# Kernel tuning notes

Hardware: AMD Instinct MI355X
Metric: run time of the kernel (lower is better)

Reference implementation:

```python
import jax, jax.numpy as jnp
import numpy as np

N_NODES = 100000
N_EDGES = 1000000
D_MODEL = 128
EDGE_DIM = 64
LN_EPS = 1e-5


def _layernorm(x, gamma, beta, eps=LN_EPS):
    mu = jnp.mean(x, axis=-1, keepdims=True)
    var = jnp.var(x, axis=-1, keepdims=True)
    return (x - mu) * jax.lax.rsqrt(var + eps) * gamma + beta


def setup_inputs() -> dict:
    key = jax.random.key(0)
    ks = jax.random.split(key, 12)
    std = 1.0 / np.sqrt(D_MODEL)
    stde = 1.0 / np.sqrt(EDGE_DIM)
    return {
        "x_src": jax.random.normal(ks[0], (N_NODES, D_MODEL), jnp.float32),
        "x_dst": jax.random.normal(ks[1], (N_NODES, D_MODEL), jnp.float32),
        "edge_attr": jax.random.normal(ks[2], (N_EDGES, EDGE_DIM), jnp.float32),
        "edge_index": jax.random.randint(ks[3], (2, N_EDGES), 0, N_NODES, jnp.int32),
        # params
        "W_src": jax.random.uniform(ks[4], (D_MODEL, D_MODEL), jnp.float32, -std, std),
        "W_dst": jax.random.uniform(ks[5], (D_MODEL, D_MODEL), jnp.float32, -std, std),
        "b_dst": jnp.zeros((D_MODEL,), jnp.float32),
        "Wg1": jax.random.uniform(ks[6], (EDGE_DIM, D_MODEL), jnp.float32, -stde, stde),
        "bg1": jnp.zeros((D_MODEL,), jnp.float32),
        "Wg2": jax.random.uniform(ks[7], (D_MODEL, 1), jnp.float32, -std, std),
        "bg2": jnp.zeros((1,), jnp.float32),
        "gamma": jnp.ones((D_MODEL,), jnp.float32),
        "beta": jnp.zeros((D_MODEL,), jnp.float32),
    }


def reference(x_src, x_dst, edge_attr, edge_index,
              W_src, W_dst, b_dst, Wg1, bg1, Wg2, bg2, gamma, beta):
    s, d = edge_index[0], edge_index[1]
    n = x_dst.shape[0]
    # gather + linear (no bias): [E, D]
    msg = x_src[s] @ W_src
    # edge gate MLP: Linear -> gelu -> Linear (no norm, eval so no dropout)
    h = jax.nn.gelu(edge_attr @ Wg1 + bg1, approximate=False)
    gate = jax.nn.sigmoid(h @ Wg2 + bg2)  # [E, 1]
    msg = msg * gate
    # scatter-add aggregate + mean by in-degree (clamped at 1)
    out = jax.ops.segment_sum(msg, d, num_segments=n)
    deg = jax.ops.segment_sum(jnp.ones((msg.shape[0],), msg.dtype), d, num_segments=n)
    out = out / jnp.clip(deg, 1.0)[:, None]
    # residual-like combine, layernorm, gelu
    out = _layernorm(out + x_dst @ W_dst + b_dst, gamma, beta)
    return jax.nn.gelu(out, approximate=False)
```

## Files before the change

### kernel.cpp

```cpp
#include <hip/hip_runtime.h>
#include <hip/hip_fp16.h>
#include <math.h>

#define N_NODES 100000
#define N_EDGES 1000000
#define D_MODEL 128
#define EDGE_DIM 64
#define SCHUNK 250
#define NSB 400

typedef short bf16x8 __attribute__((ext_vector_type(8)));
typedef float f32x4 __attribute__((ext_vector_type(4)));

__device__ __forceinline__ short f2bf(float f) {
    union { float f; unsigned u; } v; v.f = f;
    unsigned r = v.u + 0x7FFFu + ((v.u >> 16) & 1u);
    return (short)(r >> 16);
}
__device__ __forceinline__ float gelu_fast(float x) {
    float t = 0.7978845608028654f * x * (1.0f + 0.044715f * x * x);
    float e = __expf(2.0f * t);
    return x * (1.0f - __builtin_amdgcn_rcpf(e + 1.0f));
}
__device__ __forceinline__ float sigmoid_fast(float x) {
    return __builtin_amdgcn_rcpf(1.0f + __expf(-x));
}
__device__ __forceinline__ float bflo(unsigned v) { return __uint_as_float(v << 16); }
__device__ __forceinline__ float bfhi(unsigned v) { return __uint_as_float(v & 0xFFFF0000u); }

__global__ __launch_bounds__(256) void k_prep(
    const float* __restrict__ Ws, const float* __restrict__ Wd,
    const float* __restrict__ Wg1, short* __restrict__ frag,
    int* __restrict__ deg)
{
    int b = blockIdx.x;
    if (b >= 20) {
        int i = (b - 20) * 256 + threadIdx.x;
        if (i < N_NODES) deg[i] = 0;
        return;
    }
    int g = b * 256 + threadIdx.x;
    if (g >= 5120) return;
    const float* W; short* T; int q;
    if (g < 2048)      { W = Ws;  T = frag;         q = g; }
    else if (g < 4096) { W = Wd;  T = frag + 16384; q = g - 2048; }
    else               { W = Wg1; T = frag + 32768; q = g - 4096; }
    int ls = q & 63, nt = (q >> 6) & 7, kb = q >> 9;
    int col = nt * 16 + (ls & 15);
    int k0 = kb * 32 + (ls >> 4) * 8;
    bf16x8 v;
    #pragma unroll
    for (int e = 0; e < 8; ++e) v[e] = f2bf(W[(k0 + e) * D_MODEL + col]);
    *reinterpret_cast<bf16x8*>(T + (size_t)q * 8) = v;
}

__global__ void k_deg(const int* __restrict__ dst, int* __restrict__ deg, int* __restrict__ rank) {
    int e = blockIdx.x * 256 + threadIdx.x;
    if (e < N_EDGES) rank[e] = atomicAdd(&deg[dst[e]], 1);
}

__global__ __launch_bounds__(256) void k_scan1(const int* __restrict__ deg, int* __restrict__ bsum) {
    __shared__ int s[256];
    int tid = threadIdx.x;
    int i = blockIdx.x * SCHUNK + tid;
    int v = (tid < SCHUNK && i < N_NODES) ? deg[i] : 0;
    s[tid] = v; __syncthreads();
    for (int off = 128; off > 0; off >>= 1) {
        if (tid < off) s[tid] += s[tid + off];
        __syncthreads();
    }
    if (tid == 0) bsum[blockIdx.x] = s[0];
}
__global__ __launch_bounds__(512) void k_scan2(const int* __restrict__ bsum, int* __restrict__ boff) {
    __shared__ int s[512];
    int tid = threadIdx.x;
    int v = (tid < NSB) ? bsum[tid] : 0;
    s[tid] = v; __syncthreads();
    for (int off = 1; off < 512; off <<= 1) {
        int t = (tid >= off) ? s[tid - off] : 0;
        __syncthreads();
        s[tid] += t;
        __syncthreads();
    }
    if (tid < NSB) boff[tid] = s[tid] - v;
}
__global__ __launch_bounds__(256) void k_scan3(const int* __restrict__ deg, const int* __restrict__ boff,
                                               int* __restrict__ rstart) {
    __shared__ int s[256];
    int tid = threadIdx.x;
    int i = blockIdx.x * SCHUNK + tid;
    int v = (tid < SCHUNK && i < N_NODES) ? deg[i] : 0;
    s[tid] = v; __syncthreads();
    for (int off = 1; off < 256; off <<= 1) {
        int t = (tid >= off) ? s[tid - off] : 0;
        __syncthreads();
        s[tid] += t;
        __syncthreads();
    }
    int excl = s[tid] - v;
    if (tid < SCHUNK && i < N_NODES) {
        rstart[i] = boff[blockIdx.x] + excl;
        if (i == N_NODES - 1) rstart[N_NODES] = boff[blockIdx.x] + excl + v;
    }
}

__global__ __launch_bounds__(256, 3) void k_node_linear(
    const float* __restrict__ x_src, const float* __restrict__ x_dst,
    const short* __restrict__ WsrcF, const short* __restrict__ WdstF,
    const float* __restrict__ b_dst,
    short* __restrict__ ysrc, short* __restrict__ z_bf)
{
    __shared__ __align__(16) short Bf[4][8][64][8];
    const int tid = threadIdx.x;
    const int lane = tid & 63;
    const int wid = tid >> 6;
    const int l15 = lane & 15;
    const int lg = lane >> 4;
    const int mat = blockIdx.y;
    const float* __restrict__ X = mat ? x_dst : x_src;
    const short* __restrict__ WF = mat ? WdstF : WsrcF;
    const int row0 = blockIdx.x * 128 + wid * 32;

    const float* rowp[2];
    #pragma unroll
    for (int st = 0; st < 2; ++st) {
        int r = min(row0 + st * 16 + l15, N_NODES - 1);
        rowp[st] = X + (size_t)r * D_MODEL + lg * 8;
    }

    float4 buf[2][2][2];
    #pragma unroll
    for (int st = 0; st < 2; ++st) {
        buf[0][st][0] = *reinterpret_cast<const float4*>(rowp[st]);
        buf[0][st][1] = *reinterpret_cast<const float4*>(rowp[st] + 4);
    }

    #pragma unroll
    for (int i = 0; i < 8; ++i)
        reinterpret_cast<int4*>(Bf)[tid + i * 256] =
            reinterpret_cast<const int4*>(WF)[tid + i * 256];

    f32x4 acc[2][8];
    #pragma unroll
    for (int st = 0; st < 2; ++st)
        #pragma unroll
        for (int nt = 0; nt < 8; ++nt) { f32x4 zz = {0.f,0.f,0.f,0.f}; acc[st][nt] = zz; }

    __syncthreads();

    #pragma unroll
    for (int kb = 0; kb < 4; ++kb) {
        if (kb < 3) {
            #pragma unroll
            for (int st = 0; st < 2; ++st) {
                buf[(kb + 1) & 1][st][0] = *reinterpret_cast<const float4*>(rowp[st] + (kb + 1) * 32);
                buf[(kb + 1) & 1][st][1] = *reinterpret_cast<const float4*>(rowp[st] + (kb + 1) * 32 + 4);
            }
        }
        bf16x8 a[2];
        #pragma unroll
        for (int st = 0; st < 2; ++st) {
            float4 v0 = buf[kb & 1][st][0], v1 = buf[kb & 1][st][1];
            bf16x8 t;
            t[0] = f2bf(v0.x); t[1] = f2bf(v0.y); t[2] = f2bf(v0.z); t[3] = f2bf(v0.w);
            t[4] = f2bf(v1.x); t[5] = f2bf(v1.y); t[6] = f2bf(v1.z); t[7] = f2bf(v1.w);
            a[st] = t;
        }
        #pragma unroll
        for (int nt = 0; nt < 8; ++nt) {
            bf16x8 b = *reinterpret_cast<const bf16x8*>(&Bf[kb][nt][lane][0]);
            acc[0][nt] = __builtin_amdgcn_mfma_f32_16x16x32_bf16(a[0], b, acc[0][nt], 0, 0, 0);
            acc[1][nt] = __builtin_amdgcn_mfma_f32_16x16x32_bf16(a[1], b, acc[1][nt], 0, 0, 0);
        }
    }

    #pragma unroll
    for (int st = 0; st < 2; ++st) {
        int rowb = row0 + st * 16 + lg * 4;
        #pragma unroll
        for (int nt = 0; nt < 8; ++nt) {
            int col = nt * 16 + l15;
            float bias = mat ? b_dst[col] : 0.0f;
            #pragma unroll
            for (int r = 0; r < 4; ++r) {
                int row = rowb + r;
                if (row < N_NODES) {
                    float v = acc[st][nt][r];
                    if (mat) z_bf[(size_t)row * D_MODEL + col] = f2bf(v + bias);
                    else     ysrc[(size_t)row * D_MODEL + col] = f2bf(v);
                }
            }
        }
    }
}

__global__ __launch_bounds__(256, 4) void k_gate_fill(
    const float* __restrict__ ea, const short* __restrict__ Wg1F,
    const float* __restrict__ bg1, const float* __restrict__ Wg2,
    const float* __restrict__ bg2,
    const int* __restrict__ dstI, const int* __restrict__ srcI,
    const int* __restrict__ rank, const int* __restrict__ rstart,
    int2* __restrict__ sg)
{
    __shared__ __align__(16) short Bf[2][8][64][8];
    const int tid = threadIdx.x;
    const int lane = tid & 63;
    const int wid = tid >> 6;
    const int l15 = lane & 15;
    const int lg = lane >> 4;
    const int e0 = blockIdx.x * 128 + wid * 32;

    float4 av[2][2][2];
    #pragma unroll
    for (int kb = 0; kb < 2; ++kb)
        #pragma unroll
        for (int st = 0; st < 2; ++st) {
            int r = min(e0 + st * 16 + l15, N_EDGES - 1);
            const float* p = ea + (size_t)r * EDGE_DIM + kb * 32 + lg * 8;
            av[kb][st][0] = *reinterpret_cast<const float4*>(p);
            av[kb][st][1] = *reinterpret_cast<const float4*>(p + 4);
        }
    #pragma unroll
    for (int i = 0; i < 4; ++i)
        reinterpret_cast<int4*>(Bf)[tid + i * 256] =
            reinterpret_cast<const int4*>(Wg1F)[tid + i * 256];
    __syncthreads();

    bf16x8 a[2][2];
    #pragma unroll
    for (int kb = 0; kb < 2; ++kb)
        #pragma unroll
        for (int st = 0; st < 2; ++st) {
            float4 v0 = av[kb][st][0], v1 = av[kb][st][1];
            bf16x8 t;
            t[0] = f2bf(v0.x); t[1] = f2bf(v0.y); t[2] = f2bf(v0.z); t[3] = f2bf(v0.w);
            t[4] = f2bf(v1.x); t[5] = f2bf(v1.y); t[6] = f2bf(v1.z); t[7] = f2bf(v1.w);
            a[kb][st] = t;
        }

    float part[2][4] = {{0.f,0.f,0.f,0.f},{0.f,0.f,0.f,0.f}};
    #pragma unroll
    for (int ntc = 0; ntc < 2; ++ntc) {
        f32x4 acc[2][4];
        #pragma unroll
        for (int st = 0; st < 2; ++st)
            #pragma unroll
            for (int nt = 0; nt < 4; ++nt) { f32x4 zz = {0.f,0.f,0.f,0.f}; acc[st][nt] = zz; }
        #pragma unroll
        for (int kb = 0; kb < 2; ++kb)
            #pragma unroll
            for (int nt = 0; nt < 4; ++nt) {
                bf16x8 b = *reinterpret_cast<const bf16x8*>(&Bf[kb][ntc * 4 + nt][lane][0]);
                acc[0][nt] = __builtin_amdgcn_mfma_f32_16x16x32_bf16(a[kb][0], b, acc[0][nt], 0, 0, 0);
                acc[1][nt] = __builtin_amdgcn_mfma_f32_16x16x32_bf16(a[kb][1], b, acc[1][nt], 0, 0, 0);
            }
        #pragma unroll
        for (int nt = 0; nt < 4; ++nt) {
            int col = (ntc * 4 + nt) * 16 + l15;
            float b1 = bg1[col];
            float w2 = Wg2[col];
            #pragma unroll
            for (int st = 0; st < 2; ++st)
                #pragma unroll
                for (int r = 0; r < 4; ++r)
                    part[st][r] += gelu_fast(acc[st][nt][r] + b1) * w2;
        }
    }

    #pragma unroll
    for (int m = 1; m <= 8; m <<= 1)
        #pragma unroll
        for (int st = 0; st < 2; ++st)
            #pragma unroll
            for (int r = 0; r < 4; ++r)
                part[st][r] += __shfl_xor(part[st][r], m);

    if (l15 == 0) {
        float b2 = bg2[0];
        #pragma unroll
        for (int st = 0; st < 2; ++st)
            #pragma unroll
            for (int r = 0; r < 4; ++r) {
                int e = e0 + st * 16 + lg * 4 + r;
                if (e < N_EDGES) {
                    float gv = sigmoid_fast(part[st][r] + b2);
                    int d = dstI[e];
                    int p = rstart[d] + rank[e];
                    int2 v; v.x = srcI[e]; v.y = __float_as_int(gv);
                    sg[p] = v;
                }
            }
    }
}

__global__ __launch_bounds__(256) void k_agg(
    const int* __restrict__ rstart, const int2* __restrict__ sg,
    const short* __restrict__ ysrc, const short* __restrict__ z_bf,
    const float* __restrict__ gamma, const float* __restrict__ beta,
    float* __restrict__ out)
{
    const int lane = threadIdx.x & 63;
    const int wid = threadIdx.x >> 6;
    const int n = blockIdx.x * 4 + wid;
    const int start = rstart[n];
    const int end = rstart[n + 1];
    const int dg = end - start;
    const int c0 = lane * 2;

    unsigned zv = *reinterpret_cast<const unsigned*>(&z_bf[(size_t)n * D_MODEL + c0]);
    float2 gv = *reinterpret_cast<const float2*>(&gamma[c0]);
    float2 bv = *reinterpret_cast<const float2*>(&beta[c0]);

    float a0 = 0.f, a1 = 0.f;
    int t = start;
    for (; t + 4 <= end; t += 4) {
        int2 e0 = sg[t + 0];
        int2 e1 = sg[t + 1];
        int2 e2 = sg[t + 2];
        int2 e3 = sg[t + 3];
        unsigned p0 = *reinterpret_cast<const unsigned*>(&ysrc[(size_t)e0.x * D_MODEL + c0]);
        unsigned p1 = *reinterpret_cast<const unsigned*>(&ysrc[(size_t)e1.x * D_MODEL + c0]);
        unsigned p2 = *reinterpret_cast<const unsigned*>(&ysrc[(size_t)e2.x * D_MODEL + c0]);
        unsigned p3 = *reinterpret_cast<const unsigned*>(&ysrc[(size_t)e3.x * D_MODEL + c0]);
        float g0 = __int_as_float(e0.y), g1 = __int_as_float(e1.y);
        float g2 = __int_as_float(e2.y), g3 = __int_as_float(e3.y);
        a0 += g0 * bflo(p0) + g1 * bflo(p1) + g2 * bflo(p2) + g3 * bflo(p3);
        a1 += g0 * bfhi(p0) + g1 * bfhi(p1) + g2 * bfhi(p2) + g3 * bfhi(p3);
    }
    for (; t < end; ++t) {
        int2 e0 = sg[t];
        float g0 = __int_as_float(e0.y);
        unsigned p0 = *reinterpret_cast<const unsigned*>(&ysrc[(size_t)e0.x * D_MODEL + c0]);
        a0 += g0 * bflo(p0);
        a1 += g0 * bfhi(p0);
    }

    float inv = 1.0f / fmaxf((float)dg, 1.0f);
    float t0 = a0 * inv + bflo(zv);
    float t1 = a1 * inv + bfhi(zv);

    float sum = t0 + t1;
    #pragma unroll
    for (int m = 1; m <= 32; m <<= 1) sum += __shfl_xor(sum, m);
    float mu = sum * (1.0f / 128.0f);
    float d0 = t0 - mu, d1 = t1 - mu;
    float vs = d0 * d0 + d1 * d1;
    #pragma unroll
    for (int m = 1; m <= 32; m <<= 1) vs += __shfl_xor(vs, m);
    float rstd = rsqrtf(vs * (1.0f / 128.0f) + 1e-5f);

    float o0 = d0 * rstd * gv.x + bv.x;
    float o1 = d1 * rstd * gv.y + bv.y;
    float2 o = make_float2(gelu_fast(o0), gelu_fast(o1));
    *reinterpret_cast<float2*>(&out[(size_t)n * D_MODEL + c0]) = o;
}

extern "C" void kernel_launch(void* const* d_in, const int* in_sizes, int n_in,
                              void* d_out, int out_size, void* d_ws, size_t ws_size,
                              hipStream_t stream)
{
    const float* x_src = (const float*)d_in[0];
    const float* x_dst = (const float*)d_in[1];
    const float* ea    = (const float*)d_in[2];
    const int*   ei    = (const int*)d_in[3];
    const float* W_src = (const float*)d_in[4];
    const float* W_dst = (const float*)d_in[5];
    const float* b_dst = (const float*)d_in[6];
    const float* Wg1   = (const float*)d_in[7];
    const float* bg1   = (const float*)d_in[8];
    const float* Wg2   = (const float*)d_in[9];
    const float* bg2   = (const float*)d_in[10];
    const float* gamma = (const float*)d_in[11];
    const float* beta  = (const float*)d_in[12];
    const int* srcIdx = ei;
    const int* dstIdx = ei + N_EDGES;

    char* ws = (char*)d_ws;
    short* fragT  = (short*)(ws);
    short* ysrc   = (short*)(ws + 81920);
    short* z_bf   = (short*)(ws + 25681920);
    int*   deg    = (int*)(ws + 51281920);
    int*   rank   = (int*)(ws + 51681920);
    int*   rstart = (int*)(ws + 55681920);
    int2*  sg     = (int2*)(ws + 56082336);
    int*   bsum   = (int*)(ws + 64082336);
    int*   boff   = (int*)(ws + 64084000);

    float* out = (float*)d_out;

    hipLaunchKernelGGL(k_prep, dim3(411), dim3(256), 0, stream, W_src, W_dst, Wg1, fragT, deg);
    hipLaunchKernelGGL(k_deg, dim3(3907), dim3(256), 0, stream, dstIdx, deg, rank);
    hipLaunchKernelGGL(k_scan1, dim3(NSB), dim3(256), 0, stream, deg, bsum);
    hipLaunchKernelGGL(k_scan2, dim3(1), dim3(512), 0, stream, bsum, boff);
    hipLaunchKernelGGL(k_scan3, dim3(NSB), dim3(256), 0, stream, deg, boff, rstart);
    hipLaunchKernelGGL(k_node_linear, dim3(782, 2), dim3(256), 0, stream,
                       x_src, x_dst, fragT, fragT + 16384, b_dst, ysrc, z_bf);
    hipLaunchKernelGGL(k_gate_fill, dim3(7813), dim3(256), 0, stream,
                       ea, fragT + 32768, bg1, Wg2, bg2, dstIdx, srcIdx, rank, rstart, sg);
    hipLaunchKernelGGL(k_agg, dim3(N_NODES / 4), dim3(256), 0, stream,
                       rstart, sg, ysrc, z_bf, gamma, beta, out);
}
```

Baseline: 277.8 us.

## Single-block scan, 4-edge-parallel aggregation with prefetch, split gate loads

Replaces the three-kernel prefix scan over node degrees with one 1024-thread block that scans serial chunks of 98 nodes per thread, which removes two launches. The aggregation kernel now has each 16-lane group load 16 bytes (8 bf16 values) per edge, so four edges are processed in parallel per wavefront. It prefetches the next edge's row and merges the groups with cross-lane shuffles. The gate kernel splits its edge_attr loads around the weight copy to shared memory and raises its occupancy hint from 4 to 5. The single-block scan runs on only one compute unit, and its strided per-thread reads of deg are uncoalesced.

```diff
diff --git a/kernel.cpp b/kernel.cpp
--- a/kernel.cpp
+++ b/kernel.cpp
@@ -6,8 +6,6 @@
 #define N_EDGES 1000000
 #define D_MODEL 128
 #define EDGE_DIM 64
-#define SCHUNK 250
-#define NSB 400
 
 typedef short bf16x8 __attribute__((ext_vector_type(8)));
 typedef float f32x4 __attribute__((ext_vector_type(4)));
@@ -27,6 +25,12 @@
 }
 __device__ __forceinline__ float bflo(unsigned v) { return __uint_as_float(v << 16); }
 __device__ __forceinline__ float bfhi(unsigned v) { return __uint_as_float(v & 0xFFFF0000u); }
+__device__ __forceinline__ bf16x8 cvt8(float4 v0, float4 v1) {
+    bf16x8 t;
+    t[0] = f2bf(v0.x); t[1] = f2bf(v0.y); t[2] = f2bf(v0.z); t[3] = f2bf(v0.w);
+    t[4] = f2bf(v1.x); t[5] = f2bf(v1.y); t[6] = f2bf(v1.z); t[7] = f2bf(v1.w);
+    return t;
+}
 
 __global__ __launch_bounds__(256) void k_prep(
     const float* __restrict__ Ws, const float* __restrict__ Wd,
@@ -59,49 +63,30 @@
     if (e < N_EDGES) rank[e] = atomicAdd(&deg[dst[e]], 1);
 }
 
-__global__ __launch_bounds__(256) void k_scan1(const int* __restrict__ deg, int* __restrict__ bsum) {
-    __shared__ int s[256];
-    int tid = threadIdx.x;
-    int i = blockIdx.x * SCHUNK + tid;
-    int v = (tid < SCHUNK && i < N_NODES) ? deg[i] : 0;
-    s[tid] = v; __syncthreads();
-    for (int off = 128; off > 0; off >>= 1) {
-        if (tid < off) s[tid] += s[tid + off];
+#define SC_C 98
+__global__ __launch_bounds__(1024) void k_scan_single(const int* __restrict__ deg,
+                                                      int* __restrict__ rstart)
+{
+    __shared__ int s[1024];
+    const int t = threadIdx.x;
+    const int i0 = t * SC_C;
+    const int iend = min(i0 + SC_C, N_NODES);
+    int sum = 0;
+    for (int i = i0; i < iend; ++i) sum += deg[i];
+    s[t] = sum; __syncthreads();
+    #pragma unroll
+    for (int off = 1; off < 1024; off <<= 1) {
+        int v = (t >= off) ? s[t - off] : 0;
         __syncthreads();
-    }
-    if (tid == 0) bsum[blockIdx.x] = s[0];
-}
-__global__ __launch_bounds__(512) void k_scan2(const int* __restrict__ bsum, int* __restrict__ boff) {
-    __shared__ int s[512];
-    int tid = threadIdx.x;
-    int v = (tid < NSB) ? bsum[tid] : 0;
-    s[tid] = v; __syncthreads();
-    for (int off = 1; off < 512; off <<= 1) {
-        int t = (tid >= off) ? s[tid - off] : 0;
+        s[t] += v;
         __syncthreads();
-        s[tid] += t;
-        __syncthreads();
-    }
-    if (tid < NSB) boff[tid] = s[tid] - v;
-}
-__global__ __launch_bounds__(256) void k_scan3(const int* __restrict__ deg, const int* __restrict__ boff,
-                                               int* __restrict__ rstart) {
-    __shared__ int s[256];
-    int tid = threadIdx.x;
-    int i = blockIdx.x * SCHUNK + tid;
-    int v = (tid < SCHUNK && i < N_NODES) ? deg[i] : 0;
-    s[tid] = v; __syncthreads();
-    for (int off = 1; off < 256; off <<= 1) {
-        int t = (tid >= off) ? s[tid - off] : 0;
-        __syncthreads();
-        s[tid] += t;
-        __syncthreads();
-    }
-    int excl = s[tid] - v;
-    if (tid < SCHUNK && i < N_NODES) {
-        rstart[i] = boff[blockIdx.x] + excl;
-        if (i == N_NODES - 1) rstart[N_NODES] = boff[blockIdx.x] + excl + v;
-    }
+    }
+    int run = s[t] - sum;
+    for (int i = i0; i < iend; ++i) {
+        rstart[i] = run;
+        run += deg[i];
+    }
+    if (i0 < N_NODES && N_NODES <= i0 + SC_C) rstart[N_NODES] = run;
 }
 
 __global__ __launch_bounds__(256, 3) void k_node_linear(
@@ -159,13 +144,8 @@
         }
         bf16x8 a[2];
         #pragma unroll
-        for (int st = 0; st < 2; ++st) {
-            float4 v0 = buf[kb & 1][st][0], v1 = buf[kb & 1][st][1];
-            bf16x8 t;
-            t[0] = f2bf(v0.x); t[1] = f2bf(v0.y); t[2] = f2bf(v0.z); t[3] = f2bf(v0.w);
-            t[4] = f2bf(v1.x); t[5] = f2bf(v1.y); t[6] = f2bf(v1.z); t[7] = f2bf(v1.w);
-            a[st] = t;
-        }
+        for (int st = 0; st < 2; ++st)
+            a[st] = cvt8(buf[kb & 1][st][0], buf[kb & 1][st][1]);
         #pragma unroll
         for (int nt = 0; nt < 8; ++nt) {
             bf16x8 b = *reinterpret_cast<const bf16x8*>(&Bf[kb][nt][lane][0]);
@@ -194,7 +174,7 @@
     }
 }
 
-__global__ __launch_bounds__(256, 4) void k_gate_fill(
+__global__ __launch_bounds__(256, 5) void k_gate_fill(
     const float* __restrict__ ea, const short* __restrict__ Wg1F,
     const float* __restrict__ bg1, const float* __restrict__ Wg2,
     const float* __restrict__ bg2,
@@ -210,33 +190,35 @@
     const int lg = lane >> 4;
     const int e0 = blockIdx.x * 128 + wid * 32;
 
-    float4 av[2][2][2];
-    #pragma unroll
-    for (int kb = 0; kb < 2; ++kb)
-        #pragma unroll
-        for (int st = 0; st < 2; ++st) {
-            int r = min(e0 + st * 16 + l15, N_EDGES - 1);
-            const float* p = ea + (size_t)r * EDGE_DIM + kb * 32 + lg * 8;
-            av[kb][st][0] = *reinterpret_cast<const float4*>(p);
-            av[kb][st][1] = *reinterpret_cast<const float4*>(p + 4);
-        }
+    const float* rp[2];
+    #pragma unroll
+    for (int st = 0; st < 2; ++st) {
+        int r = min(e0 + st * 16 + l15, N_EDGES - 1);
+        rp[st] = ea + (size_t)r * EDGE_DIM + lg * 8;
+    }
+    float4 b0[2][2];
+    #pragma unroll
+    for (int st = 0; st < 2; ++st) {
+        b0[st][0] = *reinterpret_cast<const float4*>(rp[st]);
+        b0[st][1] = *reinterpret_cast<const float4*>(rp[st] + 4);
+    }
     #pragma unroll
     for (int i = 0; i < 4; ++i)
         reinterpret_cast<int4*>(Bf)[tid + i * 256] =
             reinterpret_cast<const int4*>(Wg1F)[tid + i * 256];
+    float4 b1[2][2];
+    #pragma unroll
+    for (int st = 0; st < 2; ++st) {
+        b1[st][0] = *reinterpret_cast<const float4*>(rp[st] + 32);
+        b1[st][1] = *reinterpret_cast<const float4*>(rp[st] + 36);
+    }
     __syncthreads();
 
-    bf16x8 a[2][2];
-    #pragma unroll
-    for (int kb = 0; kb < 2; ++kb)
-        #pragma unroll
-        for (int st = 0; st < 2; ++st) {
-            float4 v0 = av[kb][st][0], v1 = av[kb][st][1];
-            bf16x8 t;
-            t[0] = f2bf(v0.x); t[1] = f2bf(v0.y); t[2] = f2bf(v0.z); t[3] = f2bf(v0.w);
-            t[4] = f2bf(v1.x); t[5] = f2bf(v1.y); t[6] = f2bf(v1.z); t[7] = f2bf(v1.w);
-            a[kb][st] = t;
-        }
+    bf16x8 aA[2], aB[2];
+    #pragma unroll
+    for (int st = 0; st < 2; ++st) aA[st] = cvt8(b0[st][0], b0[st][1]);
+    #pragma unroll
+    for (int st = 0; st < 2; ++st) aB[st] = cvt8(b1[st][0], b1[st][1]);
 
     float part[2][4] = {{0.f,0.f,0.f,0.f},{0.f,0.f,0.f,0.f}};
     #pragma unroll
@@ -247,23 +229,27 @@
             #pragma unroll
             for (int nt = 0; nt < 4; ++nt) { f32x4 zz = {0.f,0.f,0.f,0.f}; acc[st][nt] = zz; }
         #pragma unroll
-        for (int kb = 0; kb < 2; ++kb)
-            #pragma unroll
-            for (int nt = 0; nt < 4; ++nt) {
-                bf16x8 b = *reinterpret_cast<const bf16x8*>(&Bf[kb][ntc * 4 + nt][lane][0]);
-                acc[0][nt] = __builtin_amdgcn_mfma_f32_16x16x32_bf16(a[kb][0], b, acc[0][nt], 0, 0, 0);
-                acc[1][nt] = __builtin_amdgcn_mfma_f32_16x16x32_bf16(a[kb][1], b, acc[1][nt], 0, 0, 0);
-            }
+        for (int nt = 0; nt < 4; ++nt) {
+            bf16x8 b = *reinterpret_cast<const bf16x8*>(&Bf[0][ntc * 4 + nt][lane][0]);
+            acc[0][nt] = __builtin_amdgcn_mfma_f32_16x16x32_bf16(aA[0], b, acc[0][nt], 0, 0, 0);
+            acc[1][nt] = __builtin_amdgcn_mfma_f32_16x16x32_bf16(aA[1], b, acc[1][nt], 0, 0, 0);
+        }
+        #pragma unroll
+        for (int nt = 0; nt < 4; ++nt) {
+            bf16x8 b = *reinterpret_cast<const bf16x8*>(&Bf[1][ntc * 4 + nt][lane][0]);
+            acc[0][nt] = __builtin_amdgcn_mfma_f32_16x16x32_bf16(aB[0], b, acc[0][nt], 0, 0, 0);
+            acc[1][nt] = __builtin_amdgcn_mfma_f32_16x16x32_bf16(aB[1], b, acc[1][nt], 0, 0, 0);
+        }
         #pragma unroll
         for (int nt = 0; nt < 4; ++nt) {
             int col = (ntc * 4 + nt) * 16 + l15;
-            float b1 = bg1[col];
+            float b1c = bg1[col];
             float w2 = Wg2[col];
             #pragma unroll
             for (int st = 0; st < 2; ++st)
                 #pragma unroll
                 for (int r = 0; r < 4; ++r)
-                    part[st][r] += gelu_fast(acc[st][nt][r] + b1) * w2;
+                    part[st][r] += gelu_fast(acc[st][nt][r] + b1c) * w2;
         }
     }
 
@@ -302,57 +288,91 @@
     const int lane = threadIdx.x & 63;
     const int wid = threadIdx.x >> 6;
     const int n = blockIdx.x * 4 + wid;
+    const int l15 = lane & 15;
+    const int lg = lane >> 4;
+    const int d0 = l15 * 8;
     const int start = rstart[n];
     const int end = rstart[n + 1];
     const int dg = end - start;
-    const int c0 = lane * 2;
-
-    unsigned zv = *reinterpret_cast<const unsigned*>(&z_bf[(size_t)n * D_MODEL + c0]);
-    float2 gv = *reinterpret_cast<const float2*>(&gamma[c0]);
-    float2 bv = *reinterpret_cast<const float2*>(&beta[c0]);
-
-    float a0 = 0.f, a1 = 0.f;
-    int t = start;
-    for (; t + 4 <= end; t += 4) {
-        int2 e0 = sg[t + 0];
-        int2 e1 = sg[t + 1];
-        int2 e2 = sg[t + 2];
-        int2 e3 = sg[t + 3];
-        unsigned p0 = *reinterpret_cast<const unsigned*>(&ysrc[(size_t)e0.x * D_MODEL + c0]);
-        unsigned p1 = *reinterpret_cast<const unsigned*>(&ysrc[(size_t)e1.x * D_MODEL + c0]);
-        unsigned p2 = *reinterpret_cast<const unsigned*>(&ysrc[(size_t)e2.x * D_MODEL + c0]);
-        unsigned p3 = *reinterpret_cast<const unsigned*>(&ysrc[(size_t)e3.x * D_MODEL + c0]);
-        float g0 = __int_as_float(e0.y), g1 = __int_as_float(e1.y);
-        float g2 = __int_as_float(e2.y), g3 = __int_as_float(e3.y);
-        a0 += g0 * bflo(p0) + g1 * bflo(p1) + g2 * bflo(p2) + g3 * bflo(p3);
-        a1 += g0 * bfhi(p0) + g1 * bfhi(p1) + g2 * bfhi(p2) + g3 * bfhi(p3);
-    }
-    for (; t < end; ++t) {
-        int2 e0 = sg[t];
-        float g0 = __int_as_float(e0.y);
-        unsigned p0 = *reinterpret_cast<const unsigned*>(&ysrc[(size_t)e0.x * D_MODEL + c0]);
-        a0 += g0 * bflo(p0);
-        a1 += g0 * bfhi(p0);
+
+    uint4 zv = *reinterpret_cast<const uint4*>(&z_bf[(size_t)n * D_MODEL + d0]);
+    float4 gA = *reinterpret_cast<const float4*>(&gamma[d0]);
+    float4 gB = *reinterpret_cast<const float4*>(&gamma[d0 + 4]);
+    float4 bA = *reinterpret_cast<const float4*>(&beta[d0]);
+    float4 bB = *reinterpret_cast<const float4*>(&beta[d0 + 4]);
+
+    float a[8];
+    #pragma unroll
+    for (int j = 0; j < 8; ++j) a[j] = 0.f;
+
+    int t = start + lg;
+    bool v = t < end;
+    int2 eC = make_int2(0, 0); uint4 pC = make_uint4(0, 0, 0, 0);
+    if (v) {
+        eC = sg[t];
+        pC = *reinterpret_cast<const uint4*>(&ysrc[(size_t)eC.x * D_MODEL + d0]);
+    }
+    while (v) {
+        int t2 = t + 4;
+        bool v2 = t2 < end;
+        int2 eN = make_int2(0, 0); uint4 pN = make_uint4(0, 0, 0, 0);
+        if (v2) {
+            eN = sg[t2];
+            pN = *reinterpret_cast<const uint4*>(&ysrc[(size_t)eN.x * D_MODEL + d0]);
+        }
+        float g = __int_as_float(eC.y);
+        a[0] += g * bflo(pC.x); a[1] += g * bfhi(pC.x);
+        a[2] += g * bflo(pC.y); a[3] += g * bfhi(pC.y);
+        a[4] += g * bflo(pC.z); a[5] += g * bfhi(pC.z);
+        a[6] += g * bflo(pC.w); a[7] += g * bfhi(pC.w);
+        t = t2; eC = eN; pC = pN; v = v2;
+    }
+
+    #pragma unroll
+    for (int j = 0; j < 8; ++j) {
+        a[j] += __shfl_xor(a[j], 16);
+        a[j] += __shfl_xor(a[j], 32);
     }
 
     float inv = 1.0f / fmaxf((float)dg, 1.0f);
-    float t0 = a0 * inv + bflo(zv);
-    float t1 = a1 * inv + bfhi(zv);
-
-    float sum = t0 + t1;
-    #pragma unroll
-    for (int m = 1; m <= 32; m <<= 1) sum += __shfl_xor(sum, m);
-    float mu = sum * (1.0f / 128.0f);
-    float d0 = t0 - mu, d1 = t1 - mu;
-    float vs = d0 * d0 + d1 * d1;
-    #pragma unroll
-    for (int m = 1; m <= 32; m <<= 1) vs += __shfl_xor(vs, m);
+    float tv[8];
+    tv[0] = a[0] * inv + bflo(zv.x); tv[1] = a[1] * inv + bfhi(zv.x);
+    tv[2] = a[2] * inv + bflo(zv.y); tv[3] = a[3] * inv + bfhi(zv.y);
+    tv[4] = a[4] * inv + bflo(zv.z); tv[5] = a[5] * inv + bfhi(zv.z);
+    tv[6] = a[6] * inv + bflo(zv.w); tv[7] = a[7] * inv + bfhi(zv.w);
+
+    float s = 0.f;
+    #pragma unroll
+    for (int j = 0; j < 8; ++j) s += tv[j];
+    #pragma unroll
+    for (int m = 1; m <= 8; m <<= 1) s += __shfl_xor(s, m);
+    float mu = s * (1.0f / 128.0f);
+
+    float vs = 0.f;
+    float dv[8];
+    #pragma unroll
+    for (int j = 0; j < 8; ++j) { dv[j] = tv[j] - mu; vs += dv[j] * dv[j]; }
+    #pragma unroll
+    for (int m = 1; m <= 8; m <<= 1) vs += __shfl_xor(vs, m);
     float rstd = rsqrtf(vs * (1.0f / 128.0f) + 1e-5f);
 
-    float o0 = d0 * rstd * gv.x + bv.x;
-    float o1 = d1 * rstd * gv.y + bv.y;
-    float2 o = make_float2(gelu_fast(o0), gelu_fast(o1));
-    *reinterpret_cast<float2*>(&out[(size_t)n * D_MODEL + c0]) = o;
+    float o[8];
+    o[0] = gelu_fast(dv[0] * rstd * gA.x + bA.x);
+    o[1] = gelu_fast(dv[1] * rstd * gA.y + bA.y);
+    o[2] = gelu_fast(dv[2] * rstd * gA.z + bA.z);
+    o[3] = gelu_fast(dv[3] * rstd * gA.w + bA.w);
+    o[4] = gelu_fast(dv[4] * rstd * gB.x + bB.x);
+    o[5] = gelu_fast(dv[5] * rstd * gB.y + bB.y);
+    o[6] = gelu_fast(dv[6] * rstd * gB.z + bB.z);
+    o[7] = gelu_fast(dv[7] * rstd * gB.w + bB.w);
+
+    if (lg == 0) {
+        float4 w = make_float4(o[0], o[1], o[2], o[3]);
+        *reinterpret_cast<float4*>(&out[(size_t)n * D_MODEL + d0]) = w;
+    } else if (lg == 1) {
+        float4 w = make_float4(o[4], o[5], o[6], o[7]);
+        *reinterpret_cast<float4*>(&out[(size_t)n * D_MODEL + d0 + 4]) = w;
+    }
 }
 
 extern "C" void kernel_launch(void* const* d_in, const int* in_sizes, int n_in,
@@ -383,16 +403,12 @@
     int*   rank   = (int*)(ws + 51681920);
     int*   rstart = (int*)(ws + 55681920);
     int2*  sg     = (int2*)(ws + 56082336);
-    int*   bsum   = (int*)(ws + 64082336);
-    int*   boff   = (int*)(ws + 64084000);
 
     float* out = (float*)d_out;
 
     hipLaunchKernelGGL(k_prep, dim3(411), dim3(256), 0, stream, W_src, W_dst, Wg1, fragT, deg);
     hipLaunchKernelGGL(k_deg, dim3(3907), dim3(256), 0, stream, dstIdx, deg, rank);
-    hipLaunchKernelGGL(k_scan1, dim3(NSB), dim3(256), 0, stream, deg, bsum);
-    hipLaunchKernelGGL(k_scan2, dim3(1), dim3(512), 0, stream, bsum, boff);
-    hipLaunchKernelGGL(k_scan3, dim3(NSB), dim3(256), 0, stream, deg, boff, rstart);
+    hipLaunchKernelGGL(k_scan_single, dim3(1), dim3(1024), 0, stream, deg, rstart);
     hipLaunchKernelGGL(k_node_linear, dim3(782, 2), dim3(256), 0, stream,
                        x_src, x_dst, fragT, fragT + 16384, b_dst, ysrc, z_bf);
     hipLaunchKernelGGL(k_gate_fill, dim3(7813), dim3(256), 0, stream,
```

Result: slower. 409.4 us (+47.4%).
